# Optimization experiments

Hardware: AMD Instinct MI355X
Metric: run time of the kernel (lower is better)

The kernel has to match this reference:

```python
import jax, jax.numpy as jnp
import numpy as np

N = 4096  # out_features (rows of W)
M = 4096  # in_features (cols of W)
S = 2048  # number of Givens pairs per side (= N//2)
TOKENS = 2048
EPS = 1e-8


def setup_inputs() -> dict:
    key = jax.random.key(0)
    ks = jax.random.split(key, 6)
    x = jax.random.normal(ks[0], (TOKENS, M), dtype=jnp.float32)
    W = jax.random.normal(ks[1], (N, M), dtype=jnp.float32) * (1.0 / np.sqrt(M))
    bias = jax.random.normal(ks[2], (N,), dtype=jnp.float32) * 0.02
    theta_L = 0.02 * jax.random.normal(ks[3], (S,), dtype=jnp.float32)
    theta_R = 0.02 * jax.random.normal(ks[4], (S,), dtype=jnp.float32)
    ecd_log_mag = jnp.zeros((N,), dtype=jnp.float32)
    # disjoint index pairs: (0,1),(2,3),... as produced by a permutation reshape
    pairs_L = jnp.arange(N, dtype=jnp.int64).reshape(S, 2)
    pairs_R = jnp.arange(M, dtype=jnp.int64).reshape(S, 2)
    return {"x": x, "W": W, "bias": bias, "theta_L": theta_L,
            "theta_R": theta_R, "ecd_log_mag": ecd_log_mag,
            "pairs_L": pairs_L, "pairs_R": pairs_R}


def _apply_left_rotations(W, theta, pairs):
    # Plane (Givens) rotations on disjoint row pairs of W: [S] angles, [S,2] indices
    c = jnp.cos(theta)[:, None]
    s = jnp.sin(theta)[:, None]
    i, j = pairs[:, 0], pairs[:, 1]
    ri, rj = W[i], W[j]                       # [S, M] gathers
    return W.at[i].set(c * ri - s * rj).at[j].set(s * ri + c * rj)


def _apply_right_rotations(W, theta, pairs):
    # Plane rotations on disjoint column pairs of W
    c = jnp.cos(theta)
    s = jnp.sin(theta)
    p, q = pairs[:, 0], pairs[:, 1]
    cp, cq = W[:, p], W[:, q]                 # [N, S] gathers
    return W.at[:, p].set(c * cp - s * cq).at[:, q].set(s * cp + c * cq)


def reference(x, W, bias, theta_L, theta_R, ecd_log_mag, pairs_L, pairs_R):
    # base row norms are buffers computed under no_grad from the frozen base weight
    base_row_norms = jax.lax.stop_gradient(jnp.linalg.norm(W, axis=1))  # [N]
    Wp = _apply_left_rotations(W, theta_L, pairs_L)
    Wp = _apply_right_rotations(Wp, theta_R, pairs_R)
    # magnitude rescale: row-normalize rotated weight, scale by learned magnitude
    row_norm = jnp.linalg.norm(Wp, axis=1, keepdims=True)               # [N,1]
    mag = base_row_norms * jnp.exp(ecd_log_mag)                         # [N]
    W_eff = Wp * (mag[:, None] / (row_norm + EPS))                      # [N,M]
    return x @ W_eff.T + bias                                           # [T,N]
```

## Files before the change

kernel.cpp:

```cpp
#include <hip/hip_runtime.h>
#include <hip/hip_bf16.h>


#define GK 4096
#define GN 4096
#define GT 2048
#define NPAIR 2048

typedef __bf16 bf16x8 __attribute__((ext_vector_type(8)));
typedef float  f32x4  __attribute__((ext_vector_type(4)));

static __device__ __forceinline__ unsigned short f2bf(float f) {
    union { float f; unsigned int u; } v; v.f = f;
    unsigned int r = v.u + 0x7fffu + ((v.u >> 16) & 1u);
    return (unsigned short)(r >> 16);
}
static __device__ __forceinline__ unsigned int pack2bf(float a, float b) {
    return (unsigned int)f2bf(a) | ((unsigned int)f2bf(b) << 16);
}

static __device__ __forceinline__ void sincos_poly(float t, float* s, float* c) {
    const float t2 = t * t;
    *s = t * (1.f + t2 * (-0.16666667f + t2 * 8.3333338e-3f));
    *c = 1.f + t2 * (-0.5f + t2 * (4.1666668e-2f + t2 * -1.3888889e-3f));
}

__global__ __launch_bounds__(256) void prelude(
    const float* __restrict__ W, const float* __restrict__ thL,
    const float* __restrict__ thR, const float* __restrict__ ecd,
    const float* __restrict__ x,
    unsigned short* __restrict__ Weff, unsigned short* __restrict__ Xbf)
{
    const int tid = threadIdx.x;

    if (blockIdx.x >= 2048) {
        const int cb = blockIdx.x - 2048;
        const size_t base = (size_t)cb * 512;
        const float4* X4 = (const float4*)x;
        uint4* O4 = (uint4*)Xbf;
#pragma unroll
        for (int k = 0; k < 2; k++) {
            const size_t m = base + tid + k * 256;
            const float4 a = X4[2 * m];
            const float4 b = X4[2 * m + 1];
            uint4 o;
            o.x = pack2bf(a.x, a.y);
            o.y = pack2bf(a.z, a.w);
            o.z = pack2bf(b.x, b.y);
            o.w = pack2bf(b.z, b.w);
            O4[m] = o;
        }
        return;
    }

    const int s  = blockIdx.x;
    const int i0 = 2 * s, i1 = 2 * s + 1;

    float cL, sL;
    sincos_poly(thL[s], &sL, &cL);

    float4 b0[4], b1[4];
    float s00 = 0.f, s11 = 0.f, s01 = 0.f;

    const float4* r0 = (const float4*)(W + (size_t)i0 * GK);
    const float4* r1 = (const float4*)(W + (size_t)i1 * GK);
    const float2* T2 = (const float2*)thR;

#pragma unroll
    for (int k = 0; k < 4; k++) {
        const int c4 = tid + k * 256;
        const float4 w0 = r0[c4];
        const float4 w1 = r1[c4];
        const float2 tt = T2[c4];
        float4 cs;
        sincos_poly(tt.x, &cs.y, &cs.x);
        sincos_poly(tt.y, &cs.w, &cs.z);
        s00 += w0.x * w0.x + w0.y * w0.y + w0.z * w0.z + w0.w * w0.w;
        s11 += w1.x * w1.x + w1.y * w1.y + w1.z * w1.z + w1.w * w1.w;
        s01 += w0.x * w1.x + w0.y * w1.y + w0.z * w1.z + w0.w * w1.w;
        const float a0x = cL * w0.x - sL * w1.x;
        const float a0y = cL * w0.y - sL * w1.y;
        const float a0z = cL * w0.z - sL * w1.z;
        const float a0w = cL * w0.w - sL * w1.w;
        const float a1x = sL * w0.x + cL * w1.x;
        const float a1y = sL * w0.y + cL * w1.y;
        const float a1z = sL * w0.z + cL * w1.z;
        const float a1w = sL * w0.w + cL * w1.w;
        b0[k].x = cs.x * a0x - cs.y * a0y;
        b0[k].y = cs.y * a0x + cs.x * a0y;
        b0[k].z = cs.z * a0z - cs.w * a0w;
        b0[k].w = cs.w * a0z + cs.z * a0w;
        b1[k].x = cs.x * a1x - cs.y * a1y;
        b1[k].y = cs.y * a1x + cs.x * a1y;
        b1[k].z = cs.z * a1z - cs.w * a1w;
        b1[k].w = cs.w * a1z + cs.z * a1w;
    }

#pragma unroll
    for (int off = 32; off; off >>= 1) {
        s00 += __shfl_down(s00, off);
        s11 += __shfl_down(s11, off);
        s01 += __shfl_down(s01, off);
    }
    __shared__ float red[3][4];
    __shared__ float scales[2];
    const int wave = tid >> 6, lane = tid & 63;
    if (lane == 0) { red[0][wave] = s00; red[1][wave] = s11; red[2][wave] = s01; }
    __syncthreads();
    if (tid == 0) {
        const float t0 = red[0][0] + red[0][1] + red[0][2] + red[0][3];
        const float t1 = red[1][0] + red[1][1] + red[1][2] + red[1][3];
        const float td = red[2][0] + red[2][1] + red[2][2] + red[2][3];
        const float n0 = cL * cL * t0 + sL * sL * t1 - 2.f * cL * sL * td;
        const float n1 = sL * sL * t0 + cL * cL * t1 + 2.f * cL * sL * td;
        scales[0] = sqrtf(t0) * expf(ecd[i0]) / (sqrtf(n0) + 1e-8f);
        scales[1] = sqrtf(t1) * expf(ecd[i1]) / (sqrtf(n1) + 1e-8f);
    }
    __syncthreads();
    const float sc0 = scales[0], sc1 = scales[1];

    uint2* o0 = (uint2*)(Weff + (size_t)i0 * GK);
    uint2* o1 = (uint2*)(Weff + (size_t)i1 * GK);
#pragma unroll
    for (int k = 0; k < 4; k++) {
        const int c4 = tid + k * 256;
        uint2 p0, p1;
        p0.x = pack2bf(b0[k].x * sc0, b0[k].y * sc0);
        p0.y = pack2bf(b0[k].z * sc0, b0[k].w * sc0);
        p1.x = pack2bf(b1[k].x * sc1, b1[k].y * sc1);
        p1.y = pack2bf(b1[k].z * sc1, b1[k].w * sc1);
        o0[c4] = p0;
        o1[c4] = p1;
    }
}

static __device__ __forceinline__ void glds16(const unsigned short* g, unsigned short* l) {
    __builtin_amdgcn_global_load_lds(
        (const __attribute__((address_space(1))) unsigned int*)g,
        (__attribute__((address_space(3))) unsigned int*)l, 16, 0, 0);
}

__global__ __launch_bounds__(512, 4) void gemm_bt(
    const unsigned short* __restrict__ A,
    const unsigned short* __restrict__ B,
    const float* __restrict__ bias,
    float* __restrict__ C)
{
    constexpr int BM = 128, BN = 128, BK = 64;
    constexpr int NT = GK / BK;
    __shared__ unsigned short smem[2][2][BM * BK];

    const int tid  = threadIdx.x;
    const int lane = tid & 63;
    const int wave = tid >> 6;
    const int quad = lane >> 4;
    const int l16  = lane & 15;
    const int wm   = wave >> 2;
    const int wn   = wave & 3;
    const int bm   = blockIdx.y * BM;
    const int bn   = blockIdx.x * BN;

    const int lrow = lane >> 3;
    const int jlog = (lane & 7) ^ lrow;
    const unsigned short* gA[2];
    const unsigned short* gB[2];
    int loff[2];
#pragma unroll
    for (int j = 0; j < 2; j++) {
        const int c = 2 * wave + j;
        gA[j] = A + (size_t)(bm + c * 8 + lrow) * GK + jlog * 8;
        gB[j] = B + (size_t)(bn + c * 8 + lrow) * GK + jlog * 8;
        loff[j] = c * 512 + lane * 8;
    }

#define STAGE(buf, k0) do {                                               \
    _Pragma("unroll")                                                     \
    for (int j = 0; j < 2; j++) {                                         \
        glds16(gA[j] + (k0), &smem[buf][0][loff[j]]);                     \
        glds16(gB[j] + (k0), &smem[buf][1][loff[j]]);                     \
    } } while (0)

    f32x4 acc[4][2] = {};

#define COMPUTE(b) do {                                                   \
    const unsigned short* As_ = &smem[b][0][0];                           \
    const unsigned short* Bs_ = &smem[b][1][0];                           \
    bf16x8 aF[2][4], bF[2][2];                                            \
    _Pragma("unroll")                                                     \
    for (int kk = 0; kk < 2; kk++) {                                      \
        const int ps = ((quad + 4 * kk) ^ (l16 & 7)) * 8;                 \
        _Pragma("unroll")                                                 \
        for (int i = 0; i < 4; i++)                                       \
            aF[kk][i] = *(const bf16x8*)(As_ + (wm * 64 + i * 16 + l16) * BK + ps); \
        _Pragma("unroll")                                                 \
        for (int j = 0; j < 2; j++)                                       \
            bF[kk][j] = *(const bf16x8*)(Bs_ + (wn * 32 + j * 16 + l16) * BK + ps); \
    }                                                                     \
    _Pragma("unroll")                                                     \
    for (int i = 0; i < 4; i++) {                                         \
        _Pragma("unroll")                                                 \
        for (int j = 0; j < 2; j++) {                                     \
            acc[i][j] = __builtin_amdgcn_mfma_f32_16x16x32_bf16(          \
                aF[0][i], bF[0][j], acc[i][j], 0, 0, 0);                  \
            acc[i][j] = __builtin_amdgcn_mfma_f32_16x16x32_bf16(          \
                aF[1][i], bF[1][j], acc[i][j], 0, 0, 0);                  \
        } }                                                               \
    } while (0)

    STAGE(0, 0);
    int cur = 0;
    for (int t = 0; t < NT - 1; ++t) {
        STAGE(cur ^ 1, (t + 1) * BK);
        __builtin_amdgcn_sched_barrier(0);
        asm volatile("s_waitcnt vmcnt(4)" ::: "memory");
        __builtin_amdgcn_s_barrier();
        __builtin_amdgcn_sched_barrier(0);
        COMPUTE(cur);
        __builtin_amdgcn_sched_barrier(0);
        __builtin_amdgcn_s_barrier();
        cur ^= 1;
    }
    asm volatile("s_waitcnt vmcnt(0)" ::: "memory");
    __builtin_amdgcn_s_barrier();
    __builtin_amdgcn_sched_barrier(0);
    COMPUTE(cur);

#undef STAGE
#undef COMPUTE

#pragma unroll
    for (int i = 0; i < 4; i++) {
        const int m = bm + wm * 64 + i * 16 + quad * 4;
#pragma unroll
        for (int j = 0; j < 2; j++) {
            const int n = bn + wn * 32 + j * 16 + l16;
            const float bv = bias[n];
#pragma unroll
            for (int r = 0; r < 4; r++)
                C[(size_t)(m + r) * GN + n] = acc[i][j][r] + bv;
        }
    }
}

extern "C" void kernel_launch(void* const* d_in, const int* in_sizes, int n_in,
                              void* d_out, int out_size, void* d_ws, size_t ws_size,
                              hipStream_t stream) {
    const float* x    = (const float*)d_in[0];
    const float* W    = (const float*)d_in[1];
    const float* bias = (const float*)d_in[2];
    const float* thL  = (const float*)d_in[3];
    const float* thR  = (const float*)d_in[4];
    const float* ecd  = (const float*)d_in[5];

    unsigned short* Weff = (unsigned short*)d_ws;
    unsigned short* Xbf  = (unsigned short*)((char*)d_ws + (size_t)GN * GK * 2);

    float* out = (float*)d_out;

    prelude<<<dim3(4096), dim3(256), 0, stream>>>(W, thL, thR, ecd, x, Weff, Xbf);
    gemm_bt<<<dim3(GN / 128, GT / 128), dim3(512), 0, stream>>>(Xbf, Weff, bias, out);
}
```

Measured before the change: 208.7 us.

## Split GEMM LDS staging into double-buffered A and triple-buffered B

The GEMM main loop now uses separate LDS buffers: two for A and three for B. B tiles are prefetched two K-steps ahead and A tiles one step ahead. Loads are issued after a single barrier per iteration, which removes the second barrier that closed each iteration before. This aims to hide more global-to-LDS latency and cut synchronisation cost. In exchange LDS per block grows from 64KB to 80KB, which could affect occupancy, and the vmcnt bookkeeping is more intricate.

```diff
diff --git a/kernel.cpp b/kernel.cpp
--- a/kernel.cpp
+++ b/kernel.cpp
@@ -148,7 +148,8 @@
 {
     constexpr int BM = 128, BN = 128, BK = 64;
     constexpr int NT = GK / BK;
-    __shared__ unsigned short smem[2][2][BM * BK];
+    __shared__ unsigned short sA[2][BM * BK];
+    __shared__ unsigned short sB[3][BN * BK];
 
     const int tid  = threadIdx.x;
     const int lane = tid & 63;
@@ -173,18 +174,23 @@
         loff[j] = c * 512 + lane * 8;
     }
 
-#define STAGE(buf, k0) do {                                               \
-    _Pragma("unroll")                                                     \
-    for (int j = 0; j < 2; j++) {                                         \
-        glds16(gA[j] + (k0), &smem[buf][0][loff[j]]);                     \
-        glds16(gB[j] + (k0), &smem[buf][1][loff[j]]);                     \
-    } } while (0)
+#define STAGE_A(buf, k0) do {                                             \
+    _Pragma("unroll")                                                     \
+    for (int j = 0; j < 2; j++)                                           \
+        glds16(gA[j] + (k0), &sA[buf][loff[j]]);                          \
+    } while (0)
+
+#define STAGE_B(buf, k0) do {                                             \
+    _Pragma("unroll")                                                     \
+    for (int j = 0; j < 2; j++)                                           \
+        glds16(gB[j] + (k0), &sB[buf][loff[j]]);                          \
+    } while (0)
 
     f32x4 acc[4][2] = {};
 
-#define COMPUTE(b) do {                                                   \
-    const unsigned short* As_ = &smem[b][0][0];                           \
-    const unsigned short* Bs_ = &smem[b][1][0];                           \
+#define COMPUTE(ba, bb) do {                                              \
+    const unsigned short* As_ = &sA[ba][0];                               \
+    const unsigned short* Bs_ = &sB[bb][0];                               \
     bf16x8 aF[2][4], bF[2][2];                                            \
     _Pragma("unroll")                                                     \
     for (int kk = 0; kk < 2; kk++) {                                      \
@@ -207,25 +213,33 @@
         } }                                                               \
     } while (0)
 
-    STAGE(0, 0);
-    int cur = 0;
-    for (int t = 0; t < NT - 1; ++t) {
-        STAGE(cur ^ 1, (t + 1) * BK);
-        __builtin_amdgcn_sched_barrier(0);
-        asm volatile("s_waitcnt vmcnt(4)" ::: "memory");
+    STAGE_A(0, 0);
+    STAGE_B(0, 0);
+    STAGE_B(1, BK);
+
+    int bA = 0;
+    int bB = 0, bB2 = 2;
+    for (int t = 0; t < NT; ++t) {
+        __builtin_amdgcn_sched_barrier(0);
+        if (t < NT - 1) {
+            asm volatile("s_waitcnt vmcnt(2)" ::: "memory");
+        } else {
+            asm volatile("s_waitcnt vmcnt(0)" ::: "memory");
+        }
+        __builtin_amdgcn_sched_barrier(0);
         __builtin_amdgcn_s_barrier();
         __builtin_amdgcn_sched_barrier(0);
-        COMPUTE(cur);
-        __builtin_amdgcn_sched_barrier(0);
-        __builtin_amdgcn_s_barrier();
-        cur ^= 1;
-    }
-    asm volatile("s_waitcnt vmcnt(0)" ::: "memory");
-    __builtin_amdgcn_s_barrier();
-    __builtin_amdgcn_sched_barrier(0);
-    COMPUTE(cur);
-
-#undef STAGE
+        if (t + 1 < NT) STAGE_A(bA ^ 1, (t + 1) * BK);
+        if (t + 2 < NT) STAGE_B(bB2, (t + 2) * BK);
+        __builtin_amdgcn_sched_barrier(0);
+        COMPUTE(bA, bB);
+        bA ^= 1;
+        bB  = (bB  == 2) ? 0 : bB + 1;
+        bB2 = (bB2 == 2) ? 0 : bB2 + 1;
+    }
+
+#undef STAGE_A
+#undef STAGE_B
 #undef COMPUTE
 
 #pragma unroll
```

Result: no change. 211.6 us (+1.4%).
